# Kernel optimization log

Measured on AMD Instinct MI355X. Metric: run time of the kernel, lower is better.

## Reference

```python
import jax, jax.numpy as jnp
import numpy as np

# efficient-kan defaults: grid_size=5, spline_order=3, grid_range=[-1, 1]
K_ORDER = 3
GRID_SIZE = 5
NB = GRID_SIZE + K_ORDER  # 8 spline basis functions per input feature
GRID = jnp.arange(-K_ORDER, GRID_SIZE + K_ORDER + 1, dtype=jnp.float32) * (2.0 / GRID_SIZE) - 1.0  # 12 knots on [-2.2, 2.2]


def b_splines(x):
    """Cox-de Boor B-spline basis. x: (..., in) -> (..., in, NB)."""
    g = GRID
    xe = x[..., None]
    bases = ((xe >= g[:-1]) & (xe < g[1:])).astype(x.dtype)
    for p in range(1, K_ORDER + 1):
        bases = ((xe - g[:-(p + 1)]) / (g[p:-1] - g[:-(p + 1)])) * bases[..., :-1] \
              + ((g[p + 1:] - xe) / (g[p + 1:] - g[1:-p])) * bases[..., 1:]
    return bases


def kan_linear(x, base_w, spline_w):
    # base_w: (out, in); spline_w: (out, in, NB)
    base = jnp.einsum('...i,oi->...o', jax.nn.silu(x), base_w)
    spline = jnp.einsum('...ik,oik->...o', b_splines(x), spline_w)
    return base + spline


def kan2(x, b0, s0, b1, s1):
    return kan_linear(kan_linear(x, b0, s0), b1, s1)


def pair_scores(h, b0, s0, b1, s1):
    """All-pairs concat [h_i ; h_j] -> KAN -> scalar score. h: (S, H) -> (S, S)."""
    S, H = h.shape
    q = jnp.broadcast_to(h[:, None, :], (S, S, H))
    k = jnp.broadcast_to(h[None, :, :], (S, S, H))
    pairs = jnp.concatenate([q, k], axis=-1)  # (S, S, 2H)
    return kan2(pairs, b0, s0, b1, s1)[..., 0]  # (S, S)


def setup_inputs() -> dict:
    key = jax.random.key(0)
    ks = jax.random.split(key, 32)
    S, H, KD = 192, 128, 50

    def w(k, shape, scale):
        return jax.random.normal(k, shape, dtype=jnp.float32) * scale

    inp = {
        'x': jax.random.normal(ks[0], (S, H), dtype=jnp.float32),
        'y': jax.random.normal(ks[1], (S, H), dtype=jnp.float32),
        'target': jax.random.normal(ks[2], (S, H), dtype=jnp.float32),
        'bias': w(ks[3], (1,), 0.1),
    }
    # three pairwise-attention KANs: [2H, KD, 1]
    i = 4
    for name in ('xk', 'yk', 'tk'):
        inp[f'{name}_b0'] = w(ks[i + 0], (KD, 2 * H), 0.05)
        inp[f'{name}_s0'] = w(ks[i + 1], (KD, 2 * H, NB), 0.05)
        inp[f'{name}_b1'] = w(ks[i + 2], (1, KD), 0.1)
        inp[f'{name}_s1'] = w(ks[i + 3], (1, KD, NB), 0.1)
        i += 4
    # modal fusion KAN: [3H, KD, 3]
    inp['fk_b0'] = w(ks[i + 0], (KD, 3 * H), 0.05)
    inp['fk_s0'] = w(ks[i + 1], (KD, 3 * H, NB), 0.05)
    inp['fk_b1'] = w(ks[i + 2], (3, KD), 0.1)
    inp['fk_s1'] = w(ks[i + 3], (3, KD, NB), 0.1)
    i += 4
    # output KAN "linears": [H, H]
    inp['l1_b'] = w(ks[i + 0], (H, H), 0.05)
    inp['l1_s'] = w(ks[i + 1], (H, H, NB), 0.05)
    inp['l2_b'] = w(ks[i + 2], (H, H), 0.05)
    inp['l2_s'] = w(ks[i + 3], (H, H, NB), 0.05)
    return inp


def reference(x, y, target, bias,
              xk_b0, xk_s0, xk_b1, xk_s1,
              yk_b0, yk_s0, yk_b1, yk_s1,
              tk_b0, tk_s0, tk_b1, tk_s1,
              fk_b0, fk_s0, fk_b1, fk_s1,
              l1_b, l1_s, l2_b, l2_s):
    # pairwise KAN attention matrices, one per modality (S, S)
    x_att = pair_scores(x, xk_b0, xk_s0, xk_b1, xk_s1)
    y_att = pair_scores(y, yk_b0, yk_s0, yk_b1, yk_s1)
    t_att = pair_scores(target, tk_b0, tk_s0, tk_b1, tk_s1)
    # dynamic modality weights from global mean features
    mf = jnp.concatenate([x.mean(0), y.mean(0), target.mean(0)])[None, :]  # (1, 3H)
    wts = jax.nn.softmax(kan2(mf, fk_b0, fk_s0, fk_b1, fk_s1), axis=-1)[0]  # (3,)
    fusion = wts[0] * x_att + wts[1] * y_att + wts[2] * t_att + bias[0]
    att = jax.nn.softmax(fusion, axis=-1)  # (S, S)
    tgt = att @ target  # (S, H); dropout is identity in eval
    y1 = jax.nn.relu(kan_linear(tgt, l1_b, l1_s))
    y2 = jax.nn.relu(kan_linear(y1, l2_b, l2_s))
    return y2
```

## Files before the change

kernel.cpp:

```cpp
#include <hip/hip_runtime.h>
#include <math.h>

#define SS 192
#define HH 128
#define KDIM 50

__device__ __forceinline__ void kan_phi9(float x, float* o) {
    float g[12];
#pragma unroll
    for (int i = 0; i < 12; ++i) g[i] = (float)(i - 3) * 0.4f - 1.0f;
    float b[11];
#pragma unroll
    for (int i = 0; i < 11; ++i) b[i] = (x >= g[i] && x < g[i + 1]) ? 1.0f : 0.0f;
#pragma unroll
    for (int p = 1; p <= 3; ++p) {
#pragma unroll
        for (int i = 0; i + p < 11; ++i) {
            float l = (x - g[i]) * (1.0f / (g[i + p] - g[i]));
            float r = (g[i + p + 1] - x) * (1.0f / (g[i + p + 1] - g[i + 1]));
            b[i] = l * b[i] + r * b[i + 1];
        }
    }
#pragma unroll
    for (int i = 0; i < 8; ++i) o[i] = b[i];
    o[8] = x / (1.0f + expf(-x));
}

#define WT_ELEMS   442368
#define LT_ELEMS   147456
__global__ __launch_bounds__(256) void k0_prep(
    const float* __restrict__ xb0, const float* __restrict__ xs0,
    const float* __restrict__ yb0, const float* __restrict__ ys0,
    const float* __restrict__ tb0, const float* __restrict__ ts0,
    const float* __restrict__ l1b, const float* __restrict__ l1s,
    const float* __restrict__ l2b, const float* __restrict__ l2s,
    float* __restrict__ wt, float* __restrict__ lt1, float* __restrict__ lt2)
{
    const int gid = blockIdx.x * 256 + threadIdx.x;
    if (gid < WT_ELEMS) {
        const int kk = gid & 63;
        int t = gid >> 6;
        const int n = t % 9; t /= 9;
        const int h = t & 127; t >>= 7;
        const int half = t & 1;
        const int m = t >> 1;
        const float* b0 = (m == 0) ? xb0 : (m == 1) ? yb0 : tb0;
        const float* s0 = (m == 0) ? xs0 : (m == 1) ? ys0 : ts0;
        float v = 0.f;
        if (kk < KDIM) {
            const int col = half * 128 + h;
            v = (n < 8) ? s0[(kk * 256 + col) * 8 + n] : b0[kk * 256 + col];
        }
        wt[gid] = v;
    } else {
        int idx = gid - WT_ELEMS;
        const int which = idx >= LT_ELEMS;
        if (which) idx -= LT_ELEMS;
        const float* ls = which ? l2s : l1s;
        const float* lb = which ? l2b : l1b;
        const int o = idx & 127;
        const int t = idx >> 7;
        const int n = t % 9;
        const int h = t / 9;
        const float v = (n < 8) ? ls[(o * 128 + h) * 8 + n] : lb[o * 128 + h];
        (which ? lt2 : lt1)[idx] = v;
    }
}

__global__ __launch_bounds__(256) void k1_stage(
    const float* __restrict__ x, const float* __restrict__ y, const float* __restrict__ tg,
    const float* __restrict__ wt,
    const float* __restrict__ fb0, const float* __restrict__ fs0,
    const float* __restrict__ fb1, const float* __restrict__ fs1,
    float* __restrict__ U, float* __restrict__ Vt, float* __restrict__ wts)
{
    __shared__ float lds[7168];
    const int tid = threadIdx.x;
    const int bid = blockIdx.x;
    const int lane = tid & 63, wv = tid >> 6;

    if (bid < 144) {
        const int m  = bid / 48;
        const int i0 = (bid % 48) * 4;
        const float* in = (m == 0) ? x : (m == 1) ? y : tg;

        for (int idx = tid; idx < 512; idx += 256) {
            const int r = idx >> 7, h = idx & 127;
            float ph[9];
            kan_phi9(in[(i0 + r) * HH + h], ph);
#pragma unroll
            for (int c = 0; c < 9; ++c) lds[r * 1536 + h * 12 + c] = ph[c];
        }
        __syncthreads();

        const int kk   = tid & 63;
        const int half = (tid >> 6) & 1;
        const int hh   = tid >> 7;
        const float* wp = wt + ((size_t)((m * 2 + half) * 128 + hh * 64) * 9) * 64 + kk;
        float a0 = 0.f, a1 = 0.f, a2 = 0.f, a3 = 0.f;
        for (int hl = 0; hl < 64; ++hl) {
            const float* f0 = lds + (hh * 64 + hl) * 12;
            const float* f1 = f0 + 1536;
            const float* f2 = f0 + 3072;
            const float* f3 = f0 + 4608;
            const float* wrow = wp + hl * 576;
#pragma unroll
            for (int n = 0; n < 9; ++n) {
                const float w = wrow[n * 64];
                a0 += f0[n] * w; a1 += f1[n] * w; a2 += f2[n] * w; a3 += f3[n] * w;
            }
        }
        float* part = lds + 6144;
        const int pb = ((hh * 2 + half) * 64 + kk) * 4;
        part[pb + 0] = a0; part[pb + 1] = a1; part[pb + 2] = a2; part[pb + 3] = a3;
        __syncthreads();
        if (hh == 0 && kk < KDIM) {
#pragma unroll
            for (int r = 0; r < 4; ++r) {
                const float s = part[(half * 64 + kk) * 4 + r]
                              + part[((2 + half) * 64 + kk) * 4 + r];
                if (half == 0) U[(m * SS + i0 + r) * KDIM + kk] = s;
                else           Vt[(m * KDIM + kk) * SS + i0 + r] = s;
            }
        }
    } else {
        float* mf     = lds;
        float* zpartw = lds + 384;
        float* z      = lds + 584;
        float* part3  = lds + 634;

        for (int col = tid; col < 384; col += 256) {
            const int mm = col >> 7, cc = col & 127;
            const float* in = (mm == 0) ? x : (mm == 1) ? y : tg;
            float s = 0.f;
            for (int r = 0; r < SS; ++r) s += in[r * HH + cc];
            mf[col] = s / 192.0f;
        }
        __syncthreads();
        float zp[KDIM];
#pragma unroll
        for (int k = 0; k < KDIM; ++k) zp[k] = 0.f;
        for (int f = tid; f < 384; f += 256) {
            float ph[9];
            kan_phi9(mf[f], ph);
#pragma unroll
            for (int k = 0; k < KDIM; ++k) {
                float a = ph[8] * fb0[k * 384 + f];
                const float* sw = fs0 + (size_t)(k * 384 + f) * 8;
#pragma unroll
                for (int n = 0; n < 8; ++n) a += ph[n] * sw[n];
                zp[k] += a;
            }
        }
#pragma unroll
        for (int k = 0; k < KDIM; ++k) {
            float v = zp[k];
#pragma unroll
            for (int o = 32; o > 0; o >>= 1) v += __shfl_xor(v, o);
            if (lane == 0) zpartw[k * 4 + wv] = v;
        }
        __syncthreads();
        if (tid < KDIM)
            z[tid] = zpartw[tid * 4 + 0] + zpartw[tid * 4 + 1]
                   + zpartw[tid * 4 + 2] + zpartw[tid * 4 + 3];
        __syncthreads();
        if (tid < KDIM) {
            float ph[9];
            kan_phi9(z[tid], ph);
#pragma unroll
            for (int oo = 0; oo < 3; ++oo) {
                float a = ph[8] * fb1[oo * KDIM + tid];
                const float* sw = fs1 + (oo * KDIM + tid) * 8;
#pragma unroll
                for (int n = 0; n < 8; ++n) a += ph[n] * sw[n];
                part3[oo * KDIM + tid] = a;
            }
        }
        __syncthreads();
        if (tid == 0) {
            float o0 = 0.f, o1 = 0.f, o2 = 0.f;
            for (int k = 0; k < KDIM; ++k) {
                o0 += part3[k]; o1 += part3[KDIM + k]; o2 += part3[2 * KDIM + k];
            }
            const float M  = fmaxf(o0, fmaxf(o1, o2));
            const float e0 = expf(o0 - M), e1 = expf(o1 - M), e2 = expf(o2 - M);
            const float s  = e0 + e1 + e2;
            wts[0] = e0 / s; wts[1] = e1 / s; wts[2] = e2 / s;
        }
    }
}

__global__ __launch_bounds__(576) void k2_att(
    const float* __restrict__ tg,
    const float* __restrict__ xb1, const float* __restrict__ xs1,
    const float* __restrict__ yb1, const float* __restrict__ ys1,
    const float* __restrict__ tb1, const float* __restrict__ ts1,
    const float* __restrict__ bias,
    const float* __restrict__ U, const float* __restrict__ Vt,
    const float* __restrict__ wts, float* __restrict__ out)
{
    __shared__ float spad[3 * KDIM * 14];
    __shared__ float Uls[3 * KDIM];
    __shared__ float b1ls[3 * KDIM];
    __shared__ float smpart[576];
    __shared__ float att[SS];
    __shared__ float opart[512];
    __shared__ float red[20];
    __shared__ float wb[4];
    const int tid = threadIdx.x;
    const int i   = blockIdx.x;
    const int lane = tid & 63, wv = tid >> 6;

    for (int idx = tid; idx < 3 * KDIM * 14; idx += 576) {
        const int m = idx / (KDIM * 14);
        const int r = idx % (KDIM * 14);
        const int k = r / 14, c = r % 14;
        const float* s1 = (m == 0) ? xs1 : (m == 1) ? ys1 : ts1;
        spad[idx] = (c >= 3 && c < 11) ? s1[k * 8 + (c - 3)] : 0.f;
    }
    if (tid < 3 * KDIM) {
        const int m = tid / KDIM, k = tid % KDIM;
        const float* b1 = (m == 0) ? xb1 : (m == 1) ? yb1 : tb1;
        b1ls[tid] = b1[k];
        Uls[tid]  = U[(m * SS + i) * KDIM + k];
    }
    if (tid < 3)  wb[tid] = wts[tid];
    if (tid == 3) wb[3] = bias[0];
    __syncthreads();

    {
        const int m = tid / 192, j = tid % 192;
        const float* vcol = Vt + m * KDIM * SS + j;
        const float* spm  = spad + m * KDIM * 14;
        const float* Um   = Uls + m * KDIM;
        const float* bm   = b1ls + m * KDIM;
        float sm = 0.f;
        for (int k = 0; k < KDIM; ++k) {
            const float zv  = Um[k] + vcol[k * SS];
            const float sig = 1.0f / (1.0f + expf(-zv));
            sm += zv * sig * bm[k];
            float t = (zv + 2.2f) * 2.5f;
            const bool inr = (t >= 0.0f) && (t < 11.0f);
            t = inr ? t : 0.0f;
            const int   c  = (int)t;
            const float u  = t - (float)c;
            const float u2 = u * u, u3 = u2 * u;
            const float wA = (1.0f/6.0f) * (1.0f - 3.0f*u + 3.0f*u2 - u3);
            const float wB = (1.0f/6.0f) * (3.0f*u3 - 6.0f*u2 + 4.0f);
            const float wC = (1.0f/6.0f) * (-3.0f*u3 + 3.0f*u2 + 3.0f*u + 1.0f);
            const float wD = (1.0f/6.0f) * u3;
            const float* sp = spm + k * 14 + c;
            const float spl = wA*sp[0] + wB*sp[1] + wC*sp[2] + wD*sp[3];
            sm += inr ? spl : 0.0f;
        }
        smpart[tid] = wb[m] * sm;
    }
    __syncthreads();

    float f = 0.f;
    if (tid < SS) f = wb[3] + smpart[tid] + smpart[tid + 192] + smpart[tid + 384];
    float mx = f;
#pragma unroll
    for (int o = 32; o > 0; o >>= 1) mx = fmaxf(mx, __shfl_xor(mx, o));
    if (lane == 0) red[wv] = mx;
    __syncthreads();
    mx = fmaxf(red[0], fmaxf(red[1], red[2]));
    const float p = (tid < SS) ? expf(f - mx) : 0.f;
    float sum = p;
#pragma unroll
    for (int o = 32; o > 0; o >>= 1) sum += __shfl_xor(sum, o);
    if (lane == 0) red[10 + wv] = sum;
    __syncthreads();
    sum = red[10] + red[11] + red[12];
    if (tid < SS) att[tid] = p / sum;
    __syncthreads();

    if (tid < 512) {
        const int col = tid & 127, ch = tid >> 7;
        float acc = 0.f;
        for (int jj = ch * 48; jj < ch * 48 + 48; ++jj)
            acc += att[jj] * tg[jj * HH + col];
        opart[tid] = acc;
    }
    __syncthreads();
    if (tid < HH)
        out[i * HH + tid] = opart[tid] + opart[tid + 128] + opart[tid + 256] + opart[tid + 384];
}

__global__ __launch_bounds__(256) void k3_kanlin_relu(
    const float* __restrict__ in, const float* __restrict__ lt,
    float* __restrict__ out)
{
    __shared__ float lds[3584];
    const int tid = threadIdx.x;
    const int i0  = blockIdx.x * 2;
    {
        const int r = tid >> 7, h = tid & 127;
        float ph[9];
        kan_phi9(in[(i0 + r) * HH + h], ph);
#pragma unroll
        for (int c = 0; c < 9; ++c) lds[r * 1536 + h * 12 + c] = ph[c];
    }
    __syncthreads();
    const int o  = tid & 127;
    const int hh = tid >> 7;
    const float* wp = lt + ((size_t)(hh * 64) * 9) * 128 + o;
    float a0 = 0.f, a1 = 0.f;
    for (int hl = 0; hl < 64; ++hl) {
        const float* f0 = lds + (hh * 64 + hl) * 12;
        const float* f1 = f0 + 1536;
        const float* wrow = wp + hl * 1152;
#pragma unroll
        for (int n = 0; n < 9; ++n) {
            const float w = wrow[n * 128];
            a0 += f0[n] * w; a1 += f1[n] * w;
        }
    }
    float* part = lds + 3072;
    part[((hh << 7) | o) * 2 + 0] = a0;
    part[((hh << 7) | o) * 2 + 1] = a1;
    __syncthreads();
    if (hh == 0) {
#pragma unroll
        for (int r = 0; r < 2; ++r) {
            const float s = part[o * 2 + r] + part[(128 + o) * 2 + r];
            out[(i0 + r) * HH + o] = fmaxf(s, 0.f);
        }
    }
}

extern "C" void kernel_launch(void* const* d_in, const int* in_sizes, int n_in,
                              void* d_out, int out_size, void* d_ws, size_t ws_size,
                              hipStream_t stream) {
    const float* x    = (const float*)d_in[0];
    const float* y    = (const float*)d_in[1];
    const float* tg   = (const float*)d_in[2];
    const float* bias = (const float*)d_in[3];
    const float* xb0  = (const float*)d_in[4];
    const float* xs0  = (const float*)d_in[5];
    const float* xb1  = (const float*)d_in[6];
    const float* xs1  = (const float*)d_in[7];
    const float* yb0  = (const float*)d_in[8];
    const float* ys0  = (const float*)d_in[9];
    const float* yb1  = (const float*)d_in[10];
    const float* ys1  = (const float*)d_in[11];
    const float* tb0  = (const float*)d_in[12];
    const float* ts0  = (const float*)d_in[13];
    const float* tb1  = (const float*)d_in[14];
    const float* ts1  = (const float*)d_in[15];
    const float* fb0  = (const float*)d_in[16];
    const float* fs0  = (const float*)d_in[17];
    const float* fb1  = (const float*)d_in[18];
    const float* fs1  = (const float*)d_in[19];
    const float* l1b  = (const float*)d_in[20];
    const float* l1s  = (const float*)d_in[21];
    const float* l2b  = (const float*)d_in[22];
    const float* l2s  = (const float*)d_in[23];

    float* ws   = (float*)d_ws;
    float* wt   = ws;
    float* lt1  = ws + WT_ELEMS;
    float* lt2  = lt1 + LT_ELEMS;
    float* U    = lt2 + LT_ELEMS;
    float* Vt   = U + 28800;
    float* wts  = Vt + 28800;
    float* tgt  = wts + 64;
    float* y1   = tgt + 24576;
    float* outp = (float*)d_out;

    k0_prep<<<2880, 256, 0, stream>>>(xb0, xs0, yb0, ys0, tb0, ts0,
                                      l1b, l1s, l2b, l2s, wt, lt1, lt2);
    k1_stage<<<145, 256, 0, stream>>>(x, y, tg, wt, fb0, fs0, fb1, fs1, U, Vt, wts);
    k2_att<<<SS, 576, 0, stream>>>(tg, xb1, xs1, yb1, ys1, tb1, ts1, bias,
                                   U, Vt, wts, tgt);
    k3_kanlin_relu<<<96, 256, 0, stream>>>(tgt, lt1, y1);
    k3_kanlin_relu<<<96, 256, 0, stream>>>(y1, lt2, outp);
}
```

Measured before the change: 202.9 us.

## Split fusion-weight path into its own kernel and widen stage/linear parallelism

```diff
diff --git a/kernel.cpp b/kernel.cpp
--- a/kernel.cpp
+++ b/kernel.cpp
@@ -4,6 +4,10 @@
 #define SS 192
 #define HH 128
 #define KDIM 50
+
+#define WT_ELEMS   442368
+#define LT_ELEMS   147456
+#define FT_ELEMS   221184
 
 __device__ __forceinline__ void kan_phi9(float x, float* o) {
     float g[12];
@@ -26,15 +30,15 @@
     o[8] = x / (1.0f + expf(-x));
 }
 
-#define WT_ELEMS   442368
-#define LT_ELEMS   147456
 __global__ __launch_bounds__(256) void k0_prep(
     const float* __restrict__ xb0, const float* __restrict__ xs0,
     const float* __restrict__ yb0, const float* __restrict__ ys0,
     const float* __restrict__ tb0, const float* __restrict__ ts0,
     const float* __restrict__ l1b, const float* __restrict__ l1s,
     const float* __restrict__ l2b, const float* __restrict__ l2s,
-    float* __restrict__ wt, float* __restrict__ lt1, float* __restrict__ lt2)
+    const float* __restrict__ fb0, const float* __restrict__ fs0,
+    float* __restrict__ wt, float* __restrict__ lt1, float* __restrict__ lt2,
+    float* __restrict__ ft)
 {
     const int gid = blockIdx.x * 256 + threadIdx.x;
     if (gid < WT_ELEMS) {
@@ -52,7 +56,7 @@
             v = (n < 8) ? s0[(kk * 256 + col) * 8 + n] : b0[kk * 256 + col];
         }
         wt[gid] = v;
-    } else {
+    } else if (gid < WT_ELEMS + 2 * LT_ELEMS) {
         int idx = gid - WT_ELEMS;
         const int which = idx >= LT_ELEMS;
         if (which) idx -= LT_ELEMS;
@@ -64,128 +68,144 @@
         const int h = t / 9;
         const float v = (n < 8) ? ls[(o * 128 + h) * 8 + n] : lb[o * 128 + h];
         (which ? lt2 : lt1)[idx] = v;
-    }
-}
-
-__global__ __launch_bounds__(256) void k1_stage(
+    } else {
+        const int idx = gid - WT_ELEMS - 2 * LT_ELEMS;
+        const int kk = idx & 63;
+        const int t = idx >> 6;
+        const int n = t % 9;
+        const int f = t / 9;
+        float v = 0.f;
+        if (kk < KDIM)
+            v = (n < 8) ? fs0[(kk * 384 + f) * 8 + n] : fb0[kk * 384 + f];
+        ft[idx] = v;
+    }
+}
+
+__global__ __launch_bounds__(512) void kf_fusion(
+    const float* __restrict__ x, const float* __restrict__ y, const float* __restrict__ tg,
+    const float* __restrict__ ft,
+    const float* __restrict__ fb1, const float* __restrict__ fs1,
+    float* __restrict__ wts)
+{
+    __shared__ float mfp[768];
+    __shared__ float fls[4608];
+    __shared__ float zpl[512];
+    __shared__ float z[64];
+    __shared__ float part3[3 * KDIM];
+    const int tid = threadIdx.x;
+
+    for (int idx = tid; idx < 768; idx += 512) {
+        const int rh = idx / 384, col = idx % 384;
+        const int mm = col >> 7, cc = col & 127;
+        const float* in = (mm == 0) ? x : (mm == 1) ? y : tg;
+        float s = 0.f;
+        for (int r = rh * 96; r < rh * 96 + 96; ++r) s += in[r * HH + cc];
+        mfp[col * 2 + rh] = s;
+    }
+    __syncthreads();
+    if (tid < 384) {
+        const float v = (mfp[tid * 2] + mfp[tid * 2 + 1]) * (1.0f / 192.0f);
+        float ph[9];
+        kan_phi9(v, ph);
+#pragma unroll
+        for (int c = 0; c < 9; ++c) fls[tid * 12 + c] = ph[c];
+    }
+    __syncthreads();
+    {
+        const int kk = tid & 63, fs = tid >> 6;
+        float a = 0.f;
+        for (int f = fs * 48; f < fs * 48 + 48; ++f) {
+            const float* ph = fls + f * 12;
+            const float* fw = ft + (size_t)f * 9 * 64 + kk;
+#pragma unroll
+            for (int n = 0; n < 9; ++n) a += ph[n] * fw[n * 64];
+        }
+        zpl[fs * 64 + kk] = a;
+    }
+    __syncthreads();
+    if (tid < 64) {
+        float s = 0.f;
+#pragma unroll
+        for (int q = 0; q < 8; ++q) s += zpl[q * 64 + tid];
+        z[tid] = s;
+    }
+    __syncthreads();
+    if (tid < KDIM) {
+        float ph[9];
+        kan_phi9(z[tid], ph);
+#pragma unroll
+        for (int oo = 0; oo < 3; ++oo) {
+            float a = ph[8] * fb1[oo * KDIM + tid];
+            const float* sw = fs1 + (oo * KDIM + tid) * 8;
+#pragma unroll
+            for (int n = 0; n < 8; ++n) a += ph[n] * sw[n];
+            part3[oo * KDIM + tid] = a;
+        }
+    }
+    __syncthreads();
+    if (tid == 0) {
+        float o0 = 0.f, o1 = 0.f, o2 = 0.f;
+        for (int k = 0; k < KDIM; ++k) {
+            o0 += part3[k]; o1 += part3[KDIM + k]; o2 += part3[2 * KDIM + k];
+        }
+        const float M  = fmaxf(o0, fmaxf(o1, o2));
+        const float e0 = expf(o0 - M), e1 = expf(o1 - M), e2 = expf(o2 - M);
+        const float s  = e0 + e1 + e2;
+        wts[0] = e0 / s; wts[1] = e1 / s; wts[2] = e2 / s;
+    }
+}
+
+__global__ __launch_bounds__(512) void k1_stage(
     const float* __restrict__ x, const float* __restrict__ y, const float* __restrict__ tg,
     const float* __restrict__ wt,
-    const float* __restrict__ fb0, const float* __restrict__ fs0,
-    const float* __restrict__ fb1, const float* __restrict__ fs1,
-    float* __restrict__ U, float* __restrict__ Vt, float* __restrict__ wts)
-{
-    __shared__ float lds[7168];
+    float* __restrict__ U, float* __restrict__ Vt)
+{
+    __shared__ float lds[4096];
     const int tid = threadIdx.x;
-    const int bid = blockIdx.x;
-    const int lane = tid & 63, wv = tid >> 6;
-
-    if (bid < 144) {
-        const int m  = bid / 48;
-        const int i0 = (bid % 48) * 4;
-        const float* in = (m == 0) ? x : (m == 1) ? y : tg;
-
-        for (int idx = tid; idx < 512; idx += 256) {
-            const int r = idx >> 7, h = idx & 127;
-            float ph[9];
-            kan_phi9(in[(i0 + r) * HH + h], ph);
-#pragma unroll
-            for (int c = 0; c < 9; ++c) lds[r * 1536 + h * 12 + c] = ph[c];
-        }
-        __syncthreads();
-
-        const int kk   = tid & 63;
-        const int half = (tid >> 6) & 1;
-        const int hh   = tid >> 7;
-        const float* wp = wt + ((size_t)((m * 2 + half) * 128 + hh * 64) * 9) * 64 + kk;
-        float a0 = 0.f, a1 = 0.f, a2 = 0.f, a3 = 0.f;
-        for (int hl = 0; hl < 64; ++hl) {
-            const float* f0 = lds + (hh * 64 + hl) * 12;
-            const float* f1 = f0 + 1536;
-            const float* f2 = f0 + 3072;
-            const float* f3 = f0 + 4608;
-            const float* wrow = wp + hl * 576;
-#pragma unroll
-            for (int n = 0; n < 9; ++n) {
-                const float w = wrow[n * 64];
-                a0 += f0[n] * w; a1 += f1[n] * w; a2 += f2[n] * w; a3 += f3[n] * w;
+    const int m  = blockIdx.x / 96;
+    const int i0 = (blockIdx.x % 96) * 2;
+    const float* in = (m == 0) ? x : (m == 1) ? y : tg;
+
+    if (tid < 256) {
+        const int r = tid >> 7, h = tid & 127;
+        float ph[9];
+        kan_phi9(in[(i0 + r) * HH + h], ph);
+#pragma unroll
+        for (int c = 0; c < 9; ++c) lds[r * 1536 + h * 12 + c] = ph[c];
+    }
+    __syncthreads();
+
+    const int kk   = tid & 63;
+    const int half = (tid >> 6) & 1;
+    const int hq   = tid >> 7;
+    const float* wp = wt + (size_t)(((m * 2 + half) * 128 + hq * 32) * 9) * 64 + kk;
+    float a0 = 0.f, a1 = 0.f;
+    for (int hl = 0; hl < 32; ++hl) {
+        const float* f0 = lds + (hq * 32 + hl) * 12;
+        const float* f1 = f0 + 1536;
+        const float* wrow = wp + hl * 576;
+#pragma unroll
+        for (int n = 0; n < 9; ++n) {
+            const float w = wrow[n * 64];
+            a0 += f0[n] * w; a1 += f1[n] * w;
+        }
+    }
+    float* part = lds + 3072;
+    const int pb = ((hq * 2 + half) * 64 + kk) * 2;
+    part[pb + 0] = a0; part[pb + 1] = a1;
+    __syncthreads();
+
+    if (tid < 128) {
+        const int k2 = tid & 63, hf = tid >> 6;
+        if (k2 < KDIM) {
+#pragma unroll
+            for (int r = 0; r < 2; ++r) {
+                float s = 0.f;
+#pragma unroll
+                for (int q = 0; q < 4; ++q) s += part[((q * 2 + hf) * 64 + k2) * 2 + r];
+                if (hf == 0) U[(m * SS + i0 + r) * KDIM + k2] = s;
+                else         Vt[(m * KDIM + k2) * SS + i0 + r] = s;
             }
-        }
-        float* part = lds + 6144;
-        const int pb = ((hh * 2 + half) * 64 + kk) * 4;
-        part[pb + 0] = a0; part[pb + 1] = a1; part[pb + 2] = a2; part[pb + 3] = a3;
-        __syncthreads();
-        if (hh == 0 && kk < KDIM) {
-#pragma unroll
-            for (int r = 0; r < 4; ++r) {
-                const float s = part[(half * 64 + kk) * 4 + r]
-                              + part[((2 + half) * 64 + kk) * 4 + r];
-                if (half == 0) U[(m * SS + i0 + r) * KDIM + kk] = s;
-                else           Vt[(m * KDIM + kk) * SS + i0 + r] = s;
-            }
-        }
-    } else {
-        float* mf     = lds;
-        float* zpartw = lds + 384;
-        float* z      = lds + 584;
-        float* part3  = lds + 634;
-
-        for (int col = tid; col < 384; col += 256) {
-            const int mm = col >> 7, cc = col & 127;
-            const float* in = (mm == 0) ? x : (mm == 1) ? y : tg;
-            float s = 0.f;
-            for (int r = 0; r < SS; ++r) s += in[r * HH + cc];
-            mf[col] = s / 192.0f;
-        }
-        __syncthreads();
-        float zp[KDIM];
-#pragma unroll
-        for (int k = 0; k < KDIM; ++k) zp[k] = 0.f;
-        for (int f = tid; f < 384; f += 256) {
-            float ph[9];
-            kan_phi9(mf[f], ph);
-#pragma unroll
-            for (int k = 0; k < KDIM; ++k) {
-                float a = ph[8] * fb0[k * 384 + f];
-                const float* sw = fs0 + (size_t)(k * 384 + f) * 8;
-#pragma unroll
-                for (int n = 0; n < 8; ++n) a += ph[n] * sw[n];
-                zp[k] += a;
-            }
-        }
-#pragma unroll
-        for (int k = 0; k < KDIM; ++k) {
-            float v = zp[k];
-#pragma unroll
-            for (int o = 32; o > 0; o >>= 1) v += __shfl_xor(v, o);
-            if (lane == 0) zpartw[k * 4 + wv] = v;
-        }
-        __syncthreads();
-        if (tid < KDIM)
-            z[tid] = zpartw[tid * 4 + 0] + zpartw[tid * 4 + 1]
-                   + zpartw[tid * 4 + 2] + zpartw[tid * 4 + 3];
-        __syncthreads();
-        if (tid < KDIM) {
-            float ph[9];
-            kan_phi9(z[tid], ph);
-#pragma unroll
-            for (int oo = 0; oo < 3; ++oo) {
-                float a = ph[8] * fb1[oo * KDIM + tid];
-                const float* sw = fs1 + (oo * KDIM + tid) * 8;
-#pragma unroll
-                for (int n = 0; n < 8; ++n) a += ph[n] * sw[n];
-                part3[oo * KDIM + tid] = a;
-            }
-        }
-        __syncthreads();
-        if (tid == 0) {
-            float o0 = 0.f, o1 = 0.f, o2 = 0.f;
-            for (int k = 0; k < KDIM; ++k) {
-                o0 += part3[k]; o1 += part3[KDIM + k]; o2 += part3[2 * KDIM + k];
-            }
-            const float M  = fmaxf(o0, fmaxf(o1, o2));
-            const float e0 = expf(o0 - M), e1 = expf(o1 - M), e2 = expf(o2 - M);
-            const float s  = e0 + e1 + e2;
-            wts[0] = e0 / s; wts[1] = e1 / s; wts[2] = e2 / s;
         }
     }
 }
@@ -287,45 +307,36 @@
         out[i * HH + tid] = opart[tid] + opart[tid + 128] + opart[tid + 256] + opart[tid + 384];
 }
 
-__global__ __launch_bounds__(256) void k3_kanlin_relu(
+__global__ __launch_bounds__(512) void k3_kanlin_relu(
     const float* __restrict__ in, const float* __restrict__ lt,
     float* __restrict__ out)
 {
-    __shared__ float lds[3584];
+    __shared__ float lds[2048];
     const int tid = threadIdx.x;
-    const int i0  = blockIdx.x * 2;
-    {
-        const int r = tid >> 7, h = tid & 127;
+    const int i   = blockIdx.x;
+    if (tid < 128) {
         float ph[9];
-        kan_phi9(in[(i0 + r) * HH + h], ph);
-#pragma unroll
-        for (int c = 0; c < 9; ++c) lds[r * 1536 + h * 12 + c] = ph[c];
+        kan_phi9(in[i * HH + tid], ph);
+#pragma unroll
+        for (int c = 0; c < 9; ++c) lds[tid * 12 + c] = ph[c];
     }
     __syncthreads();
     const int o  = tid & 127;
-    const int hh = tid >> 7;
-    const float* wp = lt + ((size_t)(hh * 64) * 9) * 128 + o;
-    float a0 = 0.f, a1 = 0.f;
-    for (int hl = 0; hl < 64; ++hl) {
-        const float* f0 = lds + (hh * 64 + hl) * 12;
-        const float* f1 = f0 + 1536;
+    const int hq = tid >> 7;
+    const float* wp = lt + (size_t)((hq * 32) * 9) * 128 + o;
+    float a = 0.f;
+    for (int hl = 0; hl < 32; ++hl) {
+        const float* f0 = lds + (hq * 32 + hl) * 12;
         const float* wrow = wp + hl * 1152;
 #pragma unroll
-        for (int n = 0; n < 9; ++n) {
-            const float w = wrow[n * 128];
-            a0 += f0[n] * w; a1 += f1[n] * w;
-        }
-    }
-    float* part = lds + 3072;
-    part[((hh << 7) | o) * 2 + 0] = a0;
-    part[((hh << 7) | o) * 2 + 1] = a1;
-    __syncthreads();
-    if (hh == 0) {
-#pragma unroll
-        for (int r = 0; r < 2; ++r) {
-            const float s = part[o * 2 + r] + part[(128 + o) * 2 + r];
-            out[(i0 + r) * HH + o] = fmaxf(s, 0.f);
-        }
+        for (int n = 0; n < 9; ++n) a += f0[n] * wrow[n * 128];
+    }
+    float* part = lds + 1536;
+    part[hq * 128 + o] = a;
+    __syncthreads();
+    if (tid < 128) {
+        const float s = part[tid] + part[128 + tid] + part[256 + tid] + part[384 + tid];
+        out[i * HH + tid] = fmaxf(s, 0.f);
     }
 }
 
@@ -359,20 +370,23 @@
 
     float* ws   = (float*)d_ws;
     float* wt   = ws;
-    float* lt1  = ws + WT_ELEMS;
+    float* lt1  = wt + WT_ELEMS;
     float* lt2  = lt1 + LT_ELEMS;
-    float* U    = lt2 + LT_ELEMS;
+    float* ft   = lt2 + LT_ELEMS;
+    float* U    = ft + FT_ELEMS;
     float* Vt   = U + 28800;
     float* wts  = Vt + 28800;
     float* tgt  = wts + 64;
     float* y1   = tgt + 24576;
     float* outp = (float*)d_out;
 
-    k0_prep<<<2880, 256, 0, stream>>>(xb0, xs0, yb0, ys0, tb0, ts0,
-                                      l1b, l1s, l2b, l2s, wt, lt1, lt2);
-    k1_stage<<<145, 256, 0, stream>>>(x, y, tg, wt, fb0, fs0, fb1, fs1, U, Vt, wts);
+    k0_prep<<<3744, 256, 0, stream>>>(xb0, xs0, yb0, ys0, tb0, ts0,
+                                      l1b, l1s, l2b, l2s, fb0, fs0,
+                                      wt, lt1, lt2, ft);
+    kf_fusion<<<1, 512, 0, stream>>>(x, y, tg, ft, fb1, fs1, wts);
+    k1_stage<<<288, 512, 0, stream>>>(x, y, tg, wt, U, Vt);
     k2_att<<<SS, 576, 0, stream>>>(tg, xb1, xs1, yb1, ys1, tb1, ts1, bias,
                                    U, Vt, wts, tgt);
-    k3_kanlin_relu<<<96, 256, 0, stream>>>(tgt, lt1, y1);
-    k3_kanlin_relu<<<96, 256, 0, stream>>>(y1, lt2, outp);
-}
+    k3_kanlin_relu<<<192, 512, 0, stream>>>(tgt, lt1, y1);
+    k3_kanlin_relu<<<192, 512, 0, stream>>>(y1, lt2, outp);
+}
```

New measurement: 174.3 us. 14.1% less time.
